# Kernel tuning notes

Measured on AMD Instinct MI355X. Metric: run time of the kernel, lower is better.

Reference implementation:

```python
import jax, jax.numpy as jnp
import numpy as np

THETA = 10000.0
D_K = 64
MAX_SEQ_LEN = 4096
BATCH, N_HEADS, SEQ_LEN = 4, 16, 2048


def make_rotation_table(theta, d_k, max_seq_len):
    # Faithful to generate_rotation_matrix: per position, block-diagonal of 2x2
    # rotations with angle = pos / theta**(2k/d_k) for block k.
    pos = jnp.arange(max_seq_len, dtype=jnp.float32)          # [S]
    k = jnp.arange(d_k // 2, dtype=jnp.float32)               # [d_k/2]
    inv_freq = theta ** (-2.0 * k / d_k)                      # [d_k/2]
    ang = pos[:, None] * inv_freq[None, :]                    # [S, d_k/2]
    c, s = jnp.cos(ang), jnp.sin(ang)
    ev = jnp.arange(0, d_k, 2)                                # even diag indices
    T = jnp.zeros((max_seq_len, d_k, d_k), jnp.float32)
    T = T.at[:, ev, ev].set(c)
    T = T.at[:, ev, ev + 1].set(-s)
    T = T.at[:, ev + 1, ev].set(s)
    T = T.at[:, ev + 1, ev + 1].set(c)
    return T


def setup_inputs() -> dict:
    key = jax.random.key(0)
    x = jax.random.normal(key, (BATCH, N_HEADS, SEQ_LEN, D_K), dtype=jnp.float32)
    token_positions = jnp.arange(SEQ_LEN, dtype=jnp.int32)
    rotation_table = make_rotation_table(THETA, D_K, MAX_SEQ_LEN)
    return {"x": x, "token_positions": token_positions, "rotation_table": rotation_table}


def reference(x, token_positions, rotation_table):
    # Gather per-position d_k x d_k rotation matrices, then batched matvec:
    # (R[s] @ x[..., s, :, None]).squeeze(-1)
    R = rotation_table[token_positions]                       # [S, d_k, d_k]
    return jnp.einsum('sij,bhsj->bhsi', R, x)                 # [B, H, S, d_k]
```

## Files before the change

### kernel.cpp

```cpp
#include <hip/hip_runtime.h>
#include <math.h>


#define ROPE_B 4
#define ROPE_H 16
#define ROPE_S 2048
#define ROPE_D 64
#define ROPE_D4 (ROPE_D / 4)

__device__ __forceinline__ void fast_sincos(float ang, float* sp, float* cp) {
    float r = ang * 0.15915494309189535f;
    r = r - floorf(r);
    const float a = r * 6.283185307179586f;
    *sp = __sinf(a);
    *cp = __cosf(a);
}

__global__ __launch_bounds__(256) void MyRoPE_8899172237935_kernel(
    const float* __restrict__ x,
    const int* __restrict__ token_positions,
    float* __restrict__ out)
{
    const int t = blockIdx.x * 256 + threadIdx.x;

    const float4 xv = ((const float4*)x)[t];

    const int d4 = t & (ROPE_D4 - 1);
    const int s  = (t >> 4) & (ROPE_S - 1);
    const float pos = (float)token_positions[s];

    const float NL2T_32 = -0.41524101186092029f;
    const float k0 = (float)(2 * d4);
    const float if0 = exp2f(k0 * NL2T_32);
    const float if1 = exp2f((k0 + 1.0f) * NL2T_32);

    float s0, c0, s1, c1;
    fast_sincos(pos * if0, &s0, &c0);
    fast_sincos(pos * if1, &s1, &c1);

    float4 o;
    o.x = c0 * xv.x - s0 * xv.y;
    o.y = s0 * xv.x + c0 * xv.y;
    o.z = c1 * xv.z - s1 * xv.w;
    o.w = s1 * xv.z + c1 * xv.w;
    ((float4*)out)[t] = o;
}

extern "C" void kernel_launch(void* const* d_in, const int* in_sizes, int n_in,
                              void* d_out, int out_size, void* d_ws, size_t ws_size,
                              hipStream_t stream) {
    const float* x = (const float*)d_in[0];
    const int* token_positions = (const int*)d_in[1];
    float* out = (float*)d_out;

    const int total4 = ROPE_B * ROPE_H * ROPE_S * ROPE_D4;
    MyRoPE_8899172237935_kernel<<<total4 / 256, 256, 0, stream>>>(x, token_positions, out);
}
```

Baseline: 15.59 us.

## Precompute per-position cos/sin table in a prepass and use nontemporal loads/stores

Adds a small prepass kernel that computes cos and negated sin for each position and frequency into workspace. The main kernel then reads these coefficients, which are reused across batch and heads and so mostly hit cache, instead of computing exp2 and sincos per element. Loads and stores of x and out become nontemporal. The cost is a second kernel launch plus the extra coefficient reads; the sincos math it removes may have been mostly hidden behind memory traffic.

```diff
diff --git a/kernel.cpp b/kernel.cpp
--- a/kernel.cpp
+++ b/kernel.cpp
@@ -7,6 +7,9 @@
 #define ROPE_S 2048
 #define ROPE_D 64
 #define ROPE_D4 (ROPE_D / 4)
+#define COEF4_MASK (ROPE_S * ROPE_D4 - 1)
+
+typedef float floatx4 __attribute__((ext_vector_type(4)));
 
 __device__ __forceinline__ void fast_sincos(float ang, float* sp, float* cp) {
     float r = ang * 0.15915494309189535f;
@@ -16,34 +19,41 @@
     *cp = __cosf(a);
 }
 
+__global__ __launch_bounds__(256) void rope_pack_coef(
+    const int* __restrict__ token_positions,
+    float* __restrict__ coef)
+{
+    const int j = blockIdx.x * 256 + threadIdx.x;
+    const int s = j >> 5;
+    const int k = j & 31;
+
+    const float pos = (float)token_positions[s];
+    const float NL2T_32 = -0.41524101186092029f;
+    const float inv_freq = exp2f((float)k * NL2T_32);
+
+    float sn, cs;
+    fast_sincos(pos * inv_freq, &sn, &cs);
+
+    float2 cm; cm.x = cs; cm.y = -sn;
+    *(float2*)(coef + s * ROPE_D + 2 * k) = cm;
+}
+
 __global__ __launch_bounds__(256) void MyRoPE_8899172237935_kernel(
     const float* __restrict__ x,
-    const int* __restrict__ token_positions,
+    const float* __restrict__ coef,
     float* __restrict__ out)
 {
     const int t = blockIdx.x * 256 + threadIdx.x;
 
-    const float4 xv = ((const float4*)x)[t];
+    const floatx4 xv = __builtin_nontemporal_load((const floatx4*)x + t);
+    const floatx4 cm = ((const floatx4*)coef)[t & COEF4_MASK];
 
-    const int d4 = t & (ROPE_D4 - 1);
-    const int s  = (t >> 4) & (ROPE_S - 1);
-    const float pos = (float)token_positions[s];
-
-    const float NL2T_32 = -0.41524101186092029f;
-    const float k0 = (float)(2 * d4);
-    const float if0 = exp2f(k0 * NL2T_32);
-    const float if1 = exp2f((k0 + 1.0f) * NL2T_32);
-
-    float s0, c0, s1, c1;
-    fast_sincos(pos * if0, &s0, &c0);
-    fast_sincos(pos * if1, &s1, &c1);
-
-    float4 o;
-    o.x = c0 * xv.x - s0 * xv.y;
-    o.y = s0 * xv.x + c0 * xv.y;
-    o.z = c1 * xv.z - s1 * xv.w;
-    o.w = s1 * xv.z + c1 * xv.w;
-    ((float4*)out)[t] = o;
+    floatx4 o;
+    o.x = cm.x * xv.x + cm.y * xv.y;
+    o.y = cm.x * xv.y - cm.y * xv.x;
+    o.z = cm.z * xv.z + cm.w * xv.w;
+    o.w = cm.z * xv.w - cm.w * xv.z;
+    __builtin_nontemporal_store(o, (floatx4*)out + t);
 }
 
 extern "C" void kernel_launch(void* const* d_in, const int* in_sizes, int n_in,
@@ -52,7 +62,10 @@
     const float* x = (const float*)d_in[0];
     const int* token_positions = (const int*)d_in[1];
     float* out = (float*)d_out;
+    float* coef = (float*)d_ws;
+
+    rope_pack_coef<<<(ROPE_S * 32) / 256, 256, 0, stream>>>(token_positions, coef);
 
     const int total4 = ROPE_B * ROPE_H * ROPE_S * ROPE_D4;
-    MyRoPE_8899172237935_kernel<<<total4 / 256, 256, 0, stream>>>(x, token_positions, out);
+    MyRoPE_8899172237935_kernel<<<total4 / 256, 256, 0, stream>>>(x, coef, out);
 }
```

Result: slower. 20.55 us (+31.8%).
